# Performance work log

Measured on AMD Instinct MI355X. Metric: run time of the kernel, lower is better.

The kernel has to match this reference:

```python
import jax, jax.numpy as jnp
import numpy as np

D_MODEL = 1024
N_HEADS = 16
HEAD_DIM = D_MODEL // N_HEADS
B, LQ, LK = 4, 2048, 2048


def _rope(x, cos, sin):
    # x: (B, H, L, d); cos/sin: (B, 1, L, d)
    d = x.shape[-1]
    x1, x2 = x[..., : d // 2], x[..., d // 2 :]
    rotated = jnp.concatenate([-x2, x1], axis=-1)
    return x * cos + rotated * sin


def setup_inputs() -> dict:
    key = jax.random.key(0)
    ks = jax.random.split(key, 16)
    s = 1.0 / np.sqrt(D_MODEL)
    inp = {
        "query": jax.random.normal(ks[0], (B, LQ, D_MODEL), jnp.float32),
        "key": jax.random.normal(ks[1], (B, LK, D_MODEL), jnp.float32),
        "value": jax.random.normal(ks[2], (B, LK, D_MODEL), jnp.float32),
        "cos_q": jax.random.normal(ks[3], (B, LQ, HEAD_DIM), jnp.float32),
        "sin_q": jax.random.normal(ks[4], (B, LQ, HEAD_DIM), jnp.float32),
        "cos_k": jax.random.normal(ks[5], (B, LK, HEAD_DIM), jnp.float32),
        "sin_k": jax.random.normal(ks[6], (B, LK, HEAD_DIM), jnp.float32),
        "key_padding_mask": jnp.zeros((B, LK), dtype=bool),
        "Wq": jax.random.normal(ks[7], (D_MODEL, D_MODEL), jnp.float32) * s,
        "bq": jnp.zeros((D_MODEL,), jnp.float32),
        "Wk": jax.random.normal(ks[8], (D_MODEL, D_MODEL), jnp.float32) * s,
        "bk": jnp.zeros((D_MODEL,), jnp.float32),
        "Wv": jax.random.normal(ks[9], (D_MODEL, D_MODEL), jnp.float32) * s,
        "bv": jnp.zeros((D_MODEL,), jnp.float32),
        "Wo": jax.random.normal(ks[10], (D_MODEL, D_MODEL), jnp.float32) * s,
        "bo": jnp.zeros((D_MODEL,), jnp.float32),
    }
    return inp


def reference(query, key, value, cos_q, sin_q, cos_k, sin_k, key_padding_mask,
              Wq, bq, Wk, bk, Wv, bv, Wo, bo):
    Bq, Lq, _ = query.shape
    Lk = key.shape[1]
    scale = HEAD_DIM ** -0.5

    def proj(x, W, b, L):
        # torch Linear: x @ W.T + b, then (B, L, H, d) -> (B, H, L, d)
        y = jnp.einsum('ble,de->bld', x, W) + b
        return y.reshape(Bq, L, N_HEADS, HEAD_DIM).transpose(0, 2, 1, 3)

    q = proj(query, Wq, bq, Lq)
    k = proj(key, Wk, bk, Lk)
    v = proj(value, Wv, bv, Lk)

    q = _rope(q, cos_q[:, None, :Lq, :HEAD_DIM], sin_q[:, None, :Lq, :HEAD_DIM])
    k = _rope(k, cos_k[:, None, :Lk, :HEAD_DIM], sin_k[:, None, :Lk, :HEAD_DIM])

    attn = jnp.einsum('bhqd,bhkd->bhqk', q, k) * scale
    attn = jnp.where(key_padding_mask[:, None, None, :], -jnp.inf, attn)
    attn = jax.nn.softmax(attn, axis=-1)

    out = jnp.einsum('bhqk,bhkd->bhqd', attn, v)
    out = out.transpose(0, 2, 1, 3).reshape(Bq, Lq, D_MODEL)
    return jnp.einsum('ble,de->bld', out, Wo) + bo
```

## Files before the change

### kernel.cpp

```cpp
#include <hip/hip_runtime.h>
#include <hip/hip_bf16.h>
#include <stdint.h>
#include <stddef.h>

#define B_DIM 4
#define NH    16
#define LSEQ  2048
#define HD    64
#define DM    1024
#define TOKENS (B_DIM * LSEQ)

typedef __bf16 bf16_t;
typedef __attribute__((ext_vector_type(8))) __bf16 bf16x8;
typedef __attribute__((ext_vector_type(4))) __bf16 bf16x4;
typedef __attribute__((ext_vector_type(4))) float  f32x4;

#define GLD16(gp, lp) \
  __builtin_amdgcn_global_load_lds((__attribute__((address_space(1))) void*)(gp), \
                                   (__attribute__((address_space(3))) void*)(lp), 16, 0, 0)

#define WAITV4 asm volatile("s_waitcnt vmcnt(4)" ::: "memory")
#define WAITV0 asm volatile("s_waitcnt vmcnt(0)" ::: "memory")
#define WAITL0 asm volatile("s_waitcnt lgkmcnt(0)" ::: "memory")
#define SBAR   __builtin_amdgcn_s_barrier()
#define SCHED0 __builtin_amdgcn_sched_barrier(0)

__device__ __forceinline__ f32x4 mfma_16x16x32(bf16x8 a, bf16x8 b, f32x4 c) {
  return __builtin_amdgcn_mfma_f32_16x16x32_bf16(a, b, c, 0, 0, 0);
}

__global__ __launch_bounds__(256) void prep_kernel(const float* __restrict__ q,
                                                   const float* __restrict__ k,
                                                   const float* __restrict__ v,
                                                   const float* __restrict__ Wq,
                                                   const float* __restrict__ Wk,
                                                   const float* __restrict__ Wv,
                                                   const float* __restrict__ Wo,
                                                   const float* __restrict__ cos_q,
                                                   const float* __restrict__ sin_q,
                                                   const float* __restrict__ cos_k,
                                                   const float* __restrict__ sin_k,
                                                   bf16_t* __restrict__ xdst,
                                                   bf16_t* __restrict__ wdst,
                                                   float2* __restrict__ cs) {
  const int bid = blockIdx.x;
  const int tid = threadIdx.x;
  if (bid < 24576) {
    const int s = bid >> 13, off = bid & 8191;
    const float* src = (s == 0) ? q : (s == 1) ? k : v;
    const int i = (off * 256 + tid) * 4;
    const float4 val = *(const float4*)(src + i);
    bf16x4 o;
    o[0] = (bf16_t)val.x; o[1] = (bf16_t)val.y; o[2] = (bf16_t)val.z; o[3] = (bf16_t)val.w;
    *(bf16x4*)(xdst + (size_t)s * (TOKENS * (size_t)DM) + i) = o;
  } else if (bid < 28672) {
    const int s = (bid - 24576) >> 10, off = (bid - 24576) & 1023;
    const float* src = (s == 0) ? Wq : (s == 1) ? Wk : (s == 2) ? Wv : Wo;
    const int i = (off * 256 + tid) * 4;
    const float4 val = *(const float4*)(src + i);
    bf16x4 o;
    o[0] = (bf16_t)val.x; o[1] = (bf16_t)val.y; o[2] = (bf16_t)val.z; o[3] = (bf16_t)val.w;
    *(bf16x4*)(wdst + (size_t)s * (DM * (size_t)DM) + i) = o;
  } else {
    const int s = (bid - 28672) >> 9, off = (bid - 28672) & 511;
    const float* cp = (s == 0) ? cos_q : cos_k;
    const float* sp = (s == 0) ? sin_q : sin_k;
    const int i = (off * 256 + tid) * 4;
    const float4 c4 = *(const float4*)(cp + i);
    const float4 s4 = *(const float4*)(sp + i);
    float2* d = cs + (size_t)s * (TOKENS * (size_t)HD) + i;
    d[0] = make_float2(c4.x, s4.x);
    d[1] = make_float2(c4.y, s4.y);
    d[2] = make_float2(c4.z, s4.z);
    d[3] = make_float2(c4.w, s4.w);
  }
}

#define GEMM_TILE(CUR, WAIT, PRE, KK2)                                        \
  {                                                                           \
    WAIT; SBAR; SCHED0;                                                       \
    const bf16_t* Ac = &As[CUR][0];                                           \
    const bf16_t* Bc = &Bs[CUR][0];                                           \
    bf16x8 af[4], bfr[4];                                                     \
    _Pragma("unroll") for (int i_ = 0; i_ < 4; ++i_)                          \
      af[i_] = *(const bf16x8*)(Ac + (wm + i_ * 16 + l16) * 32 + fcol);       \
    _Pragma("unroll") for (int j_ = 0; j_ < 4; ++j_)                          \
      bfr[j_] = *(const bf16x8*)(Bc + (wn + j_ * 16 + l16) * 32 + fcol);      \
    _Pragma("unroll") for (int i_ = 0; i_ < 4; ++i_)                          \
      _Pragma("unroll") for (int j_ = 0; j_ < 4; ++j_)                        \
        acc[i_][j_] = mfma_16x16x32(af[i_], bfr[j_], acc[i_][j_]);            \
    WAITL0; SBAR; SCHED0;                                                     \
    if (PRE) {                                                                \
      const int kk2_ = (KK2);                                                 \
      GLD16(Ag0 + kk2_, &As[CUR][0] + ld0);                                   \
      GLD16(Ag1 + kk2_, &As[CUR][0] + ld1);                                   \
      GLD16(Bg0 + kk2_, &Bs[CUR][0] + ld0);                                   \
      GLD16(Bg1 + kk2_, &Bs[CUR][0] + ld1);                                   \
    }                                                                         \
  }

#define GEMM_LOOP                                                             \
  GLD16(Ag0, &As[0][0] + ld0); GLD16(Ag1, &As[0][0] + ld1);                   \
  GLD16(Bg0, &Bs[0][0] + ld0); GLD16(Bg1, &Bs[0][0] + ld1);                   \
  GLD16(Ag0 + 32, &As[1][0] + ld0); GLD16(Ag1 + 32, &As[1][0] + ld1);         \
  GLD16(Bg0 + 32, &Bs[1][0] + ld0); GLD16(Bg1 + 32, &Bs[1][0] + ld1);         \
  for (int ii = 0; ii < 15; ++ii) {                                           \
    const int kk2a = ii * 64 + 64;                                            \
    GEMM_TILE(0, WAITV4, true, kk2a);                                         \
    GEMM_TILE(1, WAITV4, true, kk2a + 32);                                    \
  }                                                                           \
  GEMM_TILE(0, WAITV4, false, 0);                                             \
  GEMM_TILE(1, WAITV0, false, 0);

__global__ __launch_bounds__(256) void qkv_proj_kernel(const bf16_t* __restrict__ X,
                                                       const bf16_t* __restrict__ Wb,
                                                       const float* __restrict__ bq,
                                                       const float* __restrict__ bk,
                                                       const float* __restrict__ bv,
                                                       const float2* __restrict__ csq,
                                                       const float2* __restrict__ csk,
                                                       bf16_t* __restrict__ qtb,
                                                       bf16_t* __restrict__ ktb,
                                                       bf16_t* __restrict__ vtb) {
  __shared__ bf16_t As[2][128 * 32];
  __shared__ bf16_t Bs[2][128 * 32];
  const int z = blockIdx.z;
  const bf16_t* A  = X  + (size_t)z * TOKENS * DM;
  const bf16_t* Bw = Wb + (size_t)z * DM * DM;
  const float* bias = (z == 0) ? bq : (z == 1) ? bk : bv;

  const int tid  = threadIdx.x;
  const int wave = tid >> 6, lane = tid & 63;
  const int quad = lane >> 4, l16 = lane & 15;
  const int m0 = blockIdx.x * 128, n0 = blockIdx.y * 128;
  const int wm = (wave >> 1) * 64, wn = (wave & 1) * 64;

  f32x4 acc[4][4];
#pragma unroll
  for (int i = 0; i < 4; ++i)
#pragma unroll
    for (int j = 0; j < 4; ++j) acc[i][j] = (f32x4){0.f, 0.f, 0.f, 0.f};

  const int srow = lane >> 2;
  const int scol = ((lane & 3) ^ ((lane >> 3) & 3)) * 8;
  const int c0 = wave * 2, c1 = c0 + 1;
  const int r0 = c0 * 16 + srow, r1 = c1 * 16 + srow;
  const bf16_t* Ag0 = A  + (size_t)(m0 + r0) * DM + scol;
  const bf16_t* Ag1 = A  + (size_t)(m0 + r1) * DM + scol;
  const bf16_t* Bg0 = Bw + (size_t)(n0 + r0) * DM + scol;
  const bf16_t* Bg1 = Bw + (size_t)(n0 + r1) * DM + scol;
  const int ld0 = c0 * 512, ld1 = c1 * 512;

  const int fcol = ((quad ^ ((l16 >> 1) & 3)) << 3);

  GEMM_LOOP

  if (z < 2) {
    const float2* cst = (z == 0) ? csq : csk;
    bf16_t* out = (z == 0) ? qtb : ktb;
    const int h = (n0 + wn) >> 6;
#pragma unroll
    for (int i = 0; i < 4; ++i) {
#pragma unroll
      for (int j = 0; j < 2; ++j) {
        const int hd1 = j * 16 + l16;
        const int hd2 = hd1 + 32;
        const float bn1 = bias[n0 + wn + hd1];
        const float bn2 = bias[n0 + wn + hd2];
#pragma unroll
        for (int r = 0; r < 4; ++r) {
          const int m = m0 + wm + i * 16 + quad * 4 + r;
          const int b = m >> 11, l = m & (LSEQ - 1);
          const size_t cb = ((size_t)b * LSEQ + l) * HD;
          const float x1 = (float)(bf16_t)(acc[i][j][r] + bn1);
          const float x2 = (float)(bf16_t)(acc[i][j + 2][r] + bn2);
          const float2 cs1 = cst[cb + hd1];
          const float2 cs2 = cst[cb + hd2];
          bf16_t* dst = out + (((size_t)(b * NH + h)) * LSEQ + l) * HD;
          dst[hd1] = (bf16_t)(x1 * cs1.x - x2 * cs1.y);
          dst[hd2] = (bf16_t)(x2 * cs2.x + x1 * cs2.y);
        }
      }
    }
  } else {
#pragma unroll
    for (int i = 0; i < 4; ++i) {
      const int mb = m0 + wm + i * 16 + quad * 4;
      const int b = mb >> 11, l = mb & (LSEQ - 1);
#pragma unroll
      for (int j = 0; j < 4; ++j) {
        const int n = n0 + wn + j * 16 + l16;
        const int h = n >> 6, hd = n & (HD - 1);
        const float bn = bias[n];
        bf16x4 pk;
#pragma unroll
        for (int r = 0; r < 4; ++r) pk[r] = (bf16_t)(acc[i][j][r] + bn);
        *(bf16x4*)(vtb + (((size_t)(b * NH + h)) * HD + hd) * LSEQ + l) = pk;
      }
    }
  }
}

__global__ __launch_bounds__(256) void out_gemm_kernel(const bf16_t* __restrict__ A,
                                                       const bf16_t* __restrict__ Bw,
                                                       const float* __restrict__ bias,
                                                       float* __restrict__ out) {
  __shared__ bf16_t As[2][128 * 32];
  __shared__ bf16_t Bs[2][128 * 32];
  const int tid  = threadIdx.x;
  const int wave = tid >> 6, lane = tid & 63;
  const int quad = lane >> 4, l16 = lane & 15;
  const int m0 = blockIdx.x * 128, n0 = blockIdx.y * 128;
  const int wm = (wave >> 1) * 64, wn = (wave & 1) * 64;

  f32x4 acc[4][4];
#pragma unroll
  for (int i = 0; i < 4; ++i)
#pragma unroll
    for (int j = 0; j < 4; ++j) acc[i][j] = (f32x4){0.f, 0.f, 0.f, 0.f};

  const int srow = lane >> 2;
  const int scol = ((lane & 3) ^ ((lane >> 3) & 3)) * 8;
  const int c0 = wave * 2, c1 = c0 + 1;
  const int r0 = c0 * 16 + srow, r1 = c1 * 16 + srow;
  const bf16_t* Ag0 = A  + (size_t)(m0 + r0) * DM + scol;
  const bf16_t* Ag1 = A  + (size_t)(m0 + r1) * DM + scol;
  const bf16_t* Bg0 = Bw + (size_t)(n0 + r0) * DM + scol;
  const bf16_t* Bg1 = Bw + (size_t)(n0 + r1) * DM + scol;
  const int ld0 = c0 * 512, ld1 = c1 * 512;
  const int fcol = ((quad ^ ((l16 >> 1) & 3)) << 3);

  GEMM_LOOP

#pragma unroll
  for (int i = 0; i < 4; ++i)
#pragma unroll
    for (int j = 0; j < 4; ++j) {
      const int n  = n0 + wn + j * 16 + l16;
      const float bn = bias[n];
#pragma unroll
      for (int r = 0; r < 4; ++r) {
        const int m = m0 + wm + i * 16 + quad * 4 + r;
        out[(size_t)m * DM + n] = acc[i][j][r] + bn;
      }
    }
}

#define ATTN_TILE(K0)                                                         \
  {                                                                           \
    const bf16_t* Kc = &Kl[cur][0];                                           \
    const bf16_t* Vc = &Vl[cur][0];                                           \
    f32x4 S[2][4];                                                            \
    _Pragma("unroll") for (int j = 0; j < 4; ++j) {                           \
      const bf16x8 kb0 = *(const bf16x8*)(Kc + oA + j * 1024);                \
      const bf16x8 kb1 = *(const bf16x8*)(Kc + oB + j * 1024);                \
      _Pragma("unroll") for (int u = 0; u < 2; ++u) {                         \
        f32x4 a = (f32x4){0.f, 0.f, 0.f, 0.f};                                \
        a = mfma_16x16x32(kb0, qa[u][0], a);                                  \
        a = mfma_16x16x32(kb1, qa[u][1], a);                                  \
        _Pragma("unroll") for (int r = 0; r < 4; ++r)                         \
          S[u][j][r] = __builtin_amdgcn_exp2f(a[r] * scale_l2e);              \
      }                                                                       \
    }                                                                         \
    if (has_mask) {                                                           \
      const uint64_t mlo = *(const uint64_t*)(mrow + (K0) + quad * 8);        \
      const uint64_t mhi = *(const uint64_t*)(mrow + (K0) + 32 + quad * 8);   \
      if (!__all((mlo | mhi) == 0)) {                                         \
        _Pragma("unroll") for (int j = 0; j < 4; ++j) {                       \
          const uint64_t mm = (j & 2) ? mhi : mlo;                            \
          _Pragma("unroll") for (int r = 0; r < 4; ++r)                       \
            if ((mm >> (((j & 1) * 4 + r) * 8)) & 0xff) {                     \
              S[0][j][r] = 0.f;                                               \
              S[1][j][r] = 0.f;                                               \
            }                                                                 \
        }                                                                     \
      }                                                                       \
    }                                                                         \
    bf16x8 pa[2][2];                                                          \
    _Pragma("unroll") for (int u = 0; u < 2; ++u)                             \
      _Pragma("unroll") for (int f = 0; f < 2; ++f)                           \
        _Pragma("unroll") for (int e = 0; e < 8; ++e)                         \
          pa[u][f][e] = (bf16_t)S[u][2 * f + (e >> 2)][e & 3];                \
    _Pragma("unroll") for (int u = 0; u < 2; ++u) {                           \
      Ol[u] = mfma_16x16x32(pa[u][0], ones, Ol[u]);                           \
      Ol[u] = mfma_16x16x32(pa[u][1], ones, Ol[u]);                           \
    }                                                                         \
    _Pragma("unroll") for (int jd = 0; jd < 4; ++jd) {                        \
      const bf16x8 vb0 = *(const bf16x8*)(Vc + oA + jd * 1024);               \
      const bf16x8 vb1 = *(const bf16x8*)(Vc + oB + jd * 1024);               \
      _Pragma("unroll") for (int u = 0; u < 2; ++u) {                         \
        O[u][jd] = mfma_16x16x32(pa[u][0], vb0, O[u][jd]);                    \
        O[u][jd] = mfma_16x16x32(pa[u][1], vb1, O[u][jd]);                    \
      }                                                                       \
    }                                                                         \
  }

__global__ __launch_bounds__(256, 4) void attn_kernel(const bf16_t* __restrict__ qt,
                                                      const bf16_t* __restrict__ kt,
                                                      const bf16_t* __restrict__ vt,
                                                      const unsigned char* __restrict__ mask,
                                                      bf16_t* __restrict__ ctx) {
  __shared__ bf16_t Kl[2][64 * 64];
  __shared__ bf16_t Vl[2][64 * 64];
  __shared__ int mflag;
  const int L  = blockIdx.x + (blockIdx.y << 4);
  const int bh = ((L & 7) << 3) | ((L >> 3) & 7);
  const int q0 = (L >> 6) * 128;
  const int b = bh >> 4, h = bh & (NH - 1);
  const int tid = threadIdx.x;
  const int wave = tid >> 6, lane = tid & 63;
  const int quad = lane >> 4, l16 = lane & 15;
  const float scale_l2e = 0.125f * 1.44269504f;

  const bf16_t* kbase = kt + (size_t)bh * LSEQ * HD;
  const bf16_t* vbase = vt + (size_t)bh * HD * LSEQ;
  const unsigned char* mrow = mask + (size_t)b * LSEQ;

  if (tid == 0) mflag = 0;
  __syncthreads();
  {
    const uint64_t mw = ((const uint64_t*)mrow)[tid];
    if (mw != 0) atomicOr(&mflag, 1);
  }

  bf16x8 qa[2][2];
#pragma unroll
  for (int u = 0; u < 2; ++u) {
    const bf16_t* qrow = qt + (((size_t)bh * LSEQ) + q0 + wave * 32 + u * 16 + l16) * HD;
    qa[u][0] = *(const bf16x8*)(qrow + quad * 8);
    qa[u][1] = *(const bf16x8*)(qrow + 32 + quad * 8);
  }

  f32x4 O[2][4];
  f32x4 Ol[2];
#pragma unroll
  for (int u = 0; u < 2; ++u) {
    Ol[u] = (f32x4){0.f, 0.f, 0.f, 0.f};
#pragma unroll
    for (int j = 0; j < 4; ++j) O[u][j] = (f32x4){0.f, 0.f, 0.f, 0.f};
  }
  bf16x8 ones;
#pragma unroll
  for (int e = 0; e < 8; ++e) ones[e] = (bf16_t)1.0f;

  const int srow8 = lane >> 3;
  const int scb   = lane & 7;
  const int c0 = wave * 2, c1 = c0 + 1;
  const int p0 = c0 * 8 + srow8, p1 = p0 + 8;
  const int g0 = (scb ^ srow8) * 8;
  const int sig0 = ((p0 >> 5) << 5) | (((p0 >> 2) & 3) << 3) | (((p0 >> 4) & 1) << 2) | (p0 & 3);
  const int sig1 = ((p1 >> 5) << 5) | (((p1 >> 2) & 3) << 3) | (((p1 >> 4) & 1) << 2) | (p1 & 3);
  const int kgo0 = sig0 * HD + g0, kgo1 = sig1 * HD + g0;
  const int vgo0 = p0 * LSEQ + g0, vgo1 = p1 * LSEQ + g0;
  const int ld0 = c0 * 512, ld1 = c1 * 512;

  const int sw  = l16 & 7;
  const int oA  = l16 * 64 + ((quad ^ sw) << 3);
  const int oB  = l16 * 64 + (((quad + 4) ^ sw) << 3);

  GLD16(kbase + kgo0, &Kl[0][0] + ld0);
  GLD16(kbase + kgo1, &Kl[0][0] + ld1);
  GLD16(vbase + vgo0, &Vl[0][0] + ld0);
  GLD16(vbase + vgo1, &Vl[0][0] + ld1);
  GLD16(kbase + (size_t)64 * HD + kgo0, &Kl[1][0] + ld0);
  GLD16(kbase + (size_t)64 * HD + kgo1, &Kl[1][0] + ld1);
  GLD16(vbase + (size_t)(vgo0 + 64), &Vl[1][0] + ld0);
  GLD16(vbase + (size_t)(vgo1 + 64), &Vl[1][0] + ld1);

  WAITL0; SBAR;
  const bool has_mask = (mflag != 0);

  int cur = 0;
  for (int t = 0; t < 30; ++t) {
    WAITV4; SBAR; SCHED0;
    ATTN_TILE(t * 64);
    WAITL0; SBAR; SCHED0;
    {
      const int k0n = t * 64 + 128;
      bf16_t* Kd = &Kl[cur][0];
      bf16_t* Vd = &Vl[cur][0];
      GLD16(kbase + (size_t)k0n * HD + kgo0, Kd + ld0);
      GLD16(kbase + (size_t)k0n * HD + kgo1, Kd + ld1);
      GLD16(vbase + (size_t)(vgo0 + k0n), Vd + ld0);
      GLD16(vbase + (size_t)(vgo1 + k0n), Vd + ld1);
    }
    cur ^= 1;
  }
  WAITV4; SBAR; SCHED0;
  ATTN_TILE(30 * 64);
  cur ^= 1;
  WAITV0; SBAR; SCHED0;
  ATTN_TILE(31 * 64);

#pragma unroll
  for (int u = 0; u < 2; ++u) {
    f32x4 linv;
#pragma unroll
    for (int r = 0; r < 4; ++r) linv[r] = 1.0f / Ol[u][r];
#pragma unroll
    for (int jd = 0; jd < 4; ++jd)
#pragma unroll
      for (int r = 0; r < 4; ++r) {
        const int l = q0 + wave * 32 + u * 16 + quad * 4 + r;
        const int d = h * HD + jd * 16 + l16;
        const float o = O[u][jd][r] * linv[r];
        ctx[((size_t)b * LSEQ + l) * DM + d] = (bf16_t)o;
      }
  }
}

extern "C" void kernel_launch(void* const* d_in, const int* in_sizes, int n_in,
                              void* d_out, int out_size, void* d_ws, size_t ws_size,
                              hipStream_t stream) {
  (void)in_sizes; (void)n_in; (void)out_size; (void)ws_size;
  const float* query = (const float*)d_in[0];
  const float* key   = (const float*)d_in[1];
  const float* value = (const float*)d_in[2];
  const float* cos_q = (const float*)d_in[3];
  const float* sin_q = (const float*)d_in[4];
  const float* cos_k = (const float*)d_in[5];
  const float* sin_k = (const float*)d_in[6];
  const unsigned char* mask = (const unsigned char*)d_in[7];
  const float* Wq = (const float*)d_in[8];
  const float* bq = (const float*)d_in[9];
  const float* Wk = (const float*)d_in[10];
  const float* bk = (const float*)d_in[11];
  const float* Wv = (const float*)d_in[12];
  const float* bv = (const float*)d_in[13];
  const float* Wo = (const float*)d_in[14];
  const float* bo = (const float*)d_in[15];
  float* out = (float*)d_out;

  const size_t ACT = (size_t)TOKENS * DM;
  const size_t WEL = (size_t)DM * DM;
  const size_t CSN = (size_t)TOKENS * HD;

  bf16_t* p   = (bf16_t*)d_ws;
  bf16_t* xq  = p; p += ACT;
  bf16_t* xk  = p; p += ACT;
  bf16_t* xv  = p; p += ACT;
  bf16_t* wqb = p; p += WEL;
  bf16_t* wkb = p; p += WEL;
  bf16_t* wvb = p; p += WEL;
  bf16_t* wob = p; p += WEL;
  bf16_t* qtb = p; p += ACT;
  bf16_t* ktb = p; p += ACT;
  bf16_t* vtb = p; p += ACT;
  bf16_t* ctx = xk;
  (void)xv; (void)wkb; (void)wvb;

  float2* csq = (float2*)out;
  float2* csk = csq + CSN;

  prep_kernel<<<dim3(29696), 256, 0, stream>>>(query, key, value, Wq, Wk, Wv, Wo,
                                               cos_q, sin_q, cos_k, sin_k,
                                               xq, wqb, csq);

  qkv_proj_kernel<<<dim3(TOKENS / 128, DM / 128, 3), 256, 0, stream>>>(
      xq, wqb, bq, bk, bv, csq, csk, qtb, ktb, vtb);

  attn_kernel<<<dim3(LSEQ / 128, B_DIM * NH), 256, 0, stream>>>(qtb, ktb, vtb, mask, ctx);

  out_gemm_kernel<<<dim3(TOKENS / 128, DM / 128), 256, 0, stream>>>(ctx, wob, bo, out);
}
```

Before: 355.1 us.

## Enlarge GEMM block tile to 256x128 with 128x64 per-wave tiles

Both projection GEMMs switch from a 128x128 to a 256x128 block tile. Each wave now computes 128x64 with 8x4 MFMA accumulators, and the global-to-LDS staging is reorganised into six loads per stage with a matching vmcnt wait. This raises arithmetic intensity and cuts the number of blocks to reduce load traffic per flop. In exchange it roughly doubles accumulator registers and LDS use, with launch_bounds set to 2 blocks, and halves the grid, which may reduce occupancy and load balance across the CUs.

Result: no change. 360.3 us (+1.5%).

```diff
diff --git a/kernel.cpp b/kernel.cpp
--- a/kernel.cpp
+++ b/kernel.cpp
@@ -19,6 +19,7 @@
   __builtin_amdgcn_global_load_lds((__attribute__((address_space(1))) void*)(gp), \
                                    (__attribute__((address_space(3))) void*)(lp), 16, 0, 0)
 
+#define WAITV6 asm volatile("s_waitcnt vmcnt(6)" ::: "memory")
 #define WAITV4 asm volatile("s_waitcnt vmcnt(4)" ::: "memory")
 #define WAITV0 asm volatile("s_waitcnt vmcnt(0)" ::: "memory")
 #define WAITL0 asm volatile("s_waitcnt lgkmcnt(0)" ::: "memory")
@@ -81,77 +82,87 @@
     WAIT; SBAR; SCHED0;                                                       \
     const bf16_t* Ac = &As[CUR][0];                                           \
     const bf16_t* Bc = &Bs[CUR][0];                                           \
-    bf16x8 af[4], bfr[4];                                                     \
-    _Pragma("unroll") for (int i_ = 0; i_ < 4; ++i_)                          \
+    bf16x8 af[8], bfr[4];                                                     \
+    _Pragma("unroll") for (int i_ = 0; i_ < 8; ++i_)                          \
       af[i_] = *(const bf16x8*)(Ac + (wm + i_ * 16 + l16) * 32 + fcol);       \
     _Pragma("unroll") for (int j_ = 0; j_ < 4; ++j_)                          \
       bfr[j_] = *(const bf16x8*)(Bc + (wn + j_ * 16 + l16) * 32 + fcol);      \
-    _Pragma("unroll") for (int i_ = 0; i_ < 4; ++i_)                          \
+    _Pragma("unroll") for (int i_ = 0; i_ < 8; ++i_)                          \
       _Pragma("unroll") for (int j_ = 0; j_ < 4; ++j_)                        \
         acc[i_][j_] = mfma_16x16x32(af[i_], bfr[j_], acc[i_][j_]);            \
     WAITL0; SBAR; SCHED0;                                                     \
     if (PRE) {                                                                \
       const int kk2_ = (KK2);                                                 \
-      GLD16(Ag0 + kk2_, &As[CUR][0] + ld0);                                   \
-      GLD16(Ag1 + kk2_, &As[CUR][0] + ld1);                                   \
-      GLD16(Bg0 + kk2_, &Bs[CUR][0] + ld0);                                   \
-      GLD16(Bg1 + kk2_, &Bs[CUR][0] + ld1);                                   \
+      GLD16(Ag0 + kk2_,            &As[CUR][0] + lA0);                        \
+      GLD16(Ag0 + 64 * DM + kk2_,  &As[CUR][0] + lA1);                        \
+      GLD16(Ag0 + 128 * DM + kk2_, &As[CUR][0] + lA2);                        \
+      GLD16(Ag0 + 192 * DM + kk2_, &As[CUR][0] + lA3);                        \
+      GLD16(Bg0 + kk2_,            &Bs[CUR][0] + lB0);                        \
+      GLD16(Bg0 + 64 * DM + kk2_,  &Bs[CUR][0] + lB1);                        \
     }                                                                         \
   }
 
+#define GEMM_STAGE(BUF, KK)                                                   \
+  GLD16(Ag0 + (KK),            &As[BUF][0] + lA0);                            \
+  GLD16(Ag0 + 64 * DM + (KK),  &As[BUF][0] + lA1);                            \
+  GLD16(Ag0 + 128 * DM + (KK), &As[BUF][0] + lA2);                            \
+  GLD16(Ag0 + 192 * DM + (KK), &As[BUF][0] + lA3);                            \
+  GLD16(Bg0 + (KK),            &Bs[BUF][0] + lB0);                            \
+  GLD16(Bg0 + 64 * DM + (KK),  &Bs[BUF][0] + lB1);
+
 #define GEMM_LOOP                                                             \
-  GLD16(Ag0, &As[0][0] + ld0); GLD16(Ag1, &As[0][0] + ld1);                   \
-  GLD16(Bg0, &Bs[0][0] + ld0); GLD16(Bg1, &Bs[0][0] + ld1);                   \
-  GLD16(Ag0 + 32, &As[1][0] + ld0); GLD16(Ag1 + 32, &As[1][0] + ld1);         \
-  GLD16(Bg0 + 32, &Bs[1][0] + ld0); GLD16(Bg1 + 32, &Bs[1][0] + ld1);         \
+  GEMM_STAGE(0, 0)                                                            \
+  GEMM_STAGE(1, 32)                                                           \
   for (int ii = 0; ii < 15; ++ii) {                                           \
     const int kk2a = ii * 64 + 64;                                            \
-    GEMM_TILE(0, WAITV4, true, kk2a);                                         \
-    GEMM_TILE(1, WAITV4, true, kk2a + 32);                                    \
+    GEMM_TILE(0, WAITV6, true, kk2a);                                         \
+    GEMM_TILE(1, WAITV6, true, kk2a + 32);                                    \
   }                                                                           \
-  GEMM_TILE(0, WAITV4, false, 0);                                             \
+  GEMM_TILE(0, WAITV6, false, 0);                                             \
   GEMM_TILE(1, WAITV0, false, 0);
 
-__global__ __launch_bounds__(256) void qkv_proj_kernel(const bf16_t* __restrict__ X,
-                                                       const bf16_t* __restrict__ Wb,
-                                                       const float* __restrict__ bq,
-                                                       const float* __restrict__ bk,
-                                                       const float* __restrict__ bv,
-                                                       const float2* __restrict__ csq,
-                                                       const float2* __restrict__ csk,
-                                                       bf16_t* __restrict__ qtb,
-                                                       bf16_t* __restrict__ ktb,
-                                                       bf16_t* __restrict__ vtb) {
-  __shared__ bf16_t As[2][128 * 32];
+#define GEMM_SETUP(APTR, BPTR)                                                \
+  const int wave = tid >> 6, lane = tid & 63;                                 \
+  const int quad = lane >> 4, l16 = lane & 15;                                \
+  const int wm = (wave >> 1) * 128, wn = (wave & 1) * 64;                     \
+  const int rb = wave * 16;                                                   \
+  const int srow = rb + (lane >> 2);                                          \
+  const int scol = ((lane & 3) ^ ((lane >> 3) & 3)) * 8;                      \
+  const bf16_t* Ag0 = (APTR) + (size_t)(m0 + srow) * DM + scol;               \
+  const bf16_t* Bg0 = (BPTR) + (size_t)(n0 + srow) * DM + scol;               \
+  const int lA0 = srowlds, lA1 = srowlds + 64 * 32;                           \
+  const int lA2 = srowlds + 128 * 32, lA3 = srowlds + 192 * 32;               \
+  const int lB0 = srowlds, lB1 = srowlds + 64 * 32;                           \
+  const int fcol = ((quad ^ ((l16 >> 1) & 3)) << 3);
+
+__global__ __launch_bounds__(256, 2) void qkv_proj_kernel(const bf16_t* __restrict__ X,
+                                                          const bf16_t* __restrict__ Wb,
+                                                          const float* __restrict__ bq,
+                                                          const float* __restrict__ bk,
+                                                          const float* __restrict__ bv,
+                                                          const float2* __restrict__ csq,
+                                                          const float2* __restrict__ csk,
+                                                          bf16_t* __restrict__ qtb,
+                                                          bf16_t* __restrict__ ktb,
+                                                          bf16_t* __restrict__ vtb) {
+  __shared__ bf16_t As[2][256 * 32];
   __shared__ bf16_t Bs[2][128 * 32];
   const int z = blockIdx.z;
   const bf16_t* A  = X  + (size_t)z * TOKENS * DM;
   const bf16_t* Bw = Wb + (size_t)z * DM * DM;
   const float* bias = (z == 0) ? bq : (z == 1) ? bk : bv;
 
-  const int tid  = threadIdx.x;
-  const int wave = tid >> 6, lane = tid & 63;
-  const int quad = lane >> 4, l16 = lane & 15;
-  const int m0 = blockIdx.x * 128, n0 = blockIdx.y * 128;
-  const int wm = (wave >> 1) * 64, wn = (wave & 1) * 64;
-
-  f32x4 acc[4][4];
-#pragma unroll
-  for (int i = 0; i < 4; ++i)
+  const int tid = threadIdx.x;
+  const int m0 = blockIdx.x * 256, n0 = blockIdx.y * 128;
+  const int srowlds = (tid >> 6) * 16 * 32;
+
+  f32x4 acc[8][4];
+#pragma unroll
+  for (int i = 0; i < 8; ++i)
 #pragma unroll
     for (int j = 0; j < 4; ++j) acc[i][j] = (f32x4){0.f, 0.f, 0.f, 0.f};
 
-  const int srow = lane >> 2;
-  const int scol = ((lane & 3) ^ ((lane >> 3) & 3)) * 8;
-  const int c0 = wave * 2, c1 = c0 + 1;
-  const int r0 = c0 * 16 + srow, r1 = c1 * 16 + srow;
-  const bf16_t* Ag0 = A  + (size_t)(m0 + r0) * DM + scol;
-  const bf16_t* Ag1 = A  + (size_t)(m0 + r1) * DM + scol;
-  const bf16_t* Bg0 = Bw + (size_t)(n0 + r0) * DM + scol;
-  const bf16_t* Bg1 = Bw + (size_t)(n0 + r1) * DM + scol;
-  const int ld0 = c0 * 512, ld1 = c1 * 512;
-
-  const int fcol = ((quad ^ ((l16 >> 1) & 3)) << 3);
+  GEMM_SETUP(A, Bw)
 
   GEMM_LOOP
 
@@ -160,7 +171,7 @@
     bf16_t* out = (z == 0) ? qtb : ktb;
     const int h = (n0 + wn) >> 6;
 #pragma unroll
-    for (int i = 0; i < 4; ++i) {
+    for (int i = 0; i < 8; ++i) {
 #pragma unroll
       for (int j = 0; j < 2; ++j) {
         const int hd1 = j * 16 + l16;
@@ -184,7 +195,7 @@
     }
   } else {
 #pragma unroll
-    for (int i = 0; i < 4; ++i) {
+    for (int i = 0; i < 8; ++i) {
       const int mb = m0 + wm + i * 16 + quad * 4;
       const int b = mb >> 11, l = mb & (LSEQ - 1);
 #pragma unroll
@@ -201,39 +212,28 @@
   }
 }
 
-__global__ __launch_bounds__(256) void out_gemm_kernel(const bf16_t* __restrict__ A,
-                                                       const bf16_t* __restrict__ Bw,
-                                                       const float* __restrict__ bias,
-                                                       float* __restrict__ out) {
-  __shared__ bf16_t As[2][128 * 32];
+__global__ __launch_bounds__(256, 2) void out_gemm_kernel(const bf16_t* __restrict__ A,
+                                                          const bf16_t* __restrict__ Bw,
+                                                          const float* __restrict__ bias,
+                                                          float* __restrict__ out) {
+  __shared__ bf16_t As[2][256 * 32];
   __shared__ bf16_t Bs[2][128 * 32];
-  const int tid  = threadIdx.x;
-  const int wave = tid >> 6, lane = tid & 63;
-  const int quad = lane >> 4, l16 = lane & 15;
-  const int m0 = blockIdx.x * 128, n0 = blockIdx.y * 128;
-  const int wm = (wave >> 1) * 64, wn = (wave & 1) * 64;
-
-  f32x4 acc[4][4];
-#pragma unroll
-  for (int i = 0; i < 4; ++i)
+  const int tid = threadIdx.x;
+  const int m0 = blockIdx.x * 256, n0 = blockIdx.y * 128;
+  const int srowlds = (tid >> 6) * 16 * 32;
+
+  f32x4 acc[8][4];
+#pragma unroll
+  for (int i = 0; i < 8; ++i)
 #pragma unroll
     for (int j = 0; j < 4; ++j) acc[i][j] = (f32x4){0.f, 0.f, 0.f, 0.f};
 
-  const int srow = lane >> 2;
-  const int scol = ((lane & 3) ^ ((lane >> 3) & 3)) * 8;
-  const int c0 = wave * 2, c1 = c0 + 1;
-  const int r0 = c0 * 16 + srow, r1 = c1 * 16 + srow;
-  const bf16_t* Ag0 = A  + (size_t)(m0 + r0) * DM + scol;
-  const bf16_t* Ag1 = A  + (size_t)(m0 + r1) * DM + scol;
-  const bf16_t* Bg0 = Bw + (size_t)(n0 + r0) * DM + scol;
-  const bf16_t* Bg1 = Bw + (size_t)(n0 + r1) * DM + scol;
-  const int ld0 = c0 * 512, ld1 = c1 * 512;
-  const int fcol = ((quad ^ ((l16 >> 1) & 3)) << 3);
+  GEMM_SETUP(A, Bw)
 
   GEMM_LOOP
 
 #pragma unroll
-  for (int i = 0; i < 4; ++i)
+  for (int i = 0; i < 8; ++i)
 #pragma unroll
     for (int j = 0; j < 4; ++j) {
       const int n  = n0 + wn + j * 16 + l16;
@@ -456,10 +456,10 @@
                                                cos_q, sin_q, cos_k, sin_k,
                                                xq, wqb, csq);
 
-  qkv_proj_kernel<<<dim3(TOKENS / 128, DM / 128, 3), 256, 0, stream>>>(
+  qkv_proj_kernel<<<dim3(TOKENS / 256, DM / 128, 3), 256, 0, stream>>>(
       xq, wqb, bq, bk, bv, csq, csk, qtb, ktb, vtb);
 
   attn_kernel<<<dim3(LSEQ / 128, B_DIM * NH), 256, 0, stream>>>(qtb, ktb, vtb, mask, ctx);
 
-  out_gemm_kernel<<<dim3(TOKENS / 128, DM / 128), 256, 0, stream>>>(ctx, wob, bo, out);
-}
+  out_gemm_kernel<<<dim3(TOKENS / 256, DM / 128), 256, 0, stream>>>(ctx, wob, bo, out);
+}
```
